# Performance work log

Hardware: AMD Instinct MI355X
Metric: run time of the kernel (lower is better)

The kernel has to match this reference:

```python
import jax, jax.numpy as jnp
import numpy as np

ANG = 5  # angRes; n = ANG*ANG
EPS = 1e-12  # torch F.normalize eps

def _l2norm(x, axis):
    n = jnp.sqrt(jnp.sum(x * x, axis=axis, keepdims=True))
    return x / jnp.maximum(n, EPS)

def setup_inputs() -> dict:
    key = jax.random.key(0)
    kq, kk, kv = jax.random.split(key, 3)
    shape = (16, 16, 25, 16, 128)  # b c n h w
    return {
        "token_q": jax.random.normal(kq, shape, dtype=jnp.float32),
        "token_k": jax.random.normal(kk, shape, dtype=jnp.float32),
        "token_v": jax.random.normal(kv, shape, dtype=jnp.float32),
    }

def reference(token_q, token_k, token_v):
    b, c, n, h, w = token_q.shape
    u = v = ANG
    buffer = token_v

    def to_q(x):  # b c (u v) h w -> b (c h) (w u v)
        return x.reshape(b, c, u, v, h, w).transpose(0, 1, 4, 5, 2, 3).reshape(b, c * h, w * u * v)

    def to_k(x):  # b c (u v) h w -> b (w u v) (c h)
        return x.reshape(b, c, u, v, h, w).transpose(0, 5, 2, 3, 1, 4).reshape(b, w * u * v, c * h)

    unfold_q = _l2norm(to_q(token_q), axis=-1)      # [b, ch, wuv]
    unfold_k = _l2norm(to_k(token_k), axis=-2)      # [b, wuv, ch]
    unfold_v = to_q(token_v)                        # [b, ch, wuv]

    att = jnp.einsum('bts,bsr->btr', unfold_q, unfold_k)  # [b, ch, ch]
    size = c * h
    causal = jnp.tril(jnp.ones((size, size), dtype=bool))
    att = jnp.where(causal, att, jnp.float32(-1e15))
    att = jax.nn.softmax(att, axis=-1)

    out = jnp.einsum('btr,brs->bts', att, unfold_v)  # [b, ch, wuv]
    # b (c h) (w u v) -> b c (u v) h w
    out = out.reshape(b, c, h, w, u, v).transpose(0, 1, 4, 5, 2, 3).reshape(b, c, n, h, w)
    return out + buffer
```

## Files before the change

kernel.cpp:

```cpp
#include <hip/hip_runtime.h>
#include <math.h>

#define SB 819200
#define SC 51200
#define SN 2048
#define CH 256
#define NW 3200
#define NPARTS 10
#define PARTLEN 320
#define SPART 1048576

typedef __bf16 bf16x8 __attribute__((ext_vector_type(8)));
typedef float  f32x4  __attribute__((ext_vector_type(4)));

__device__ __forceinline__ bf16x8 cvt8(float4 a, float4 b) {
    bf16x8 r;
    r[0] = (__bf16)a.x; r[1] = (__bf16)a.y; r[2] = (__bf16)a.z; r[3] = (__bf16)a.w;
    r[4] = (__bf16)b.x; r[5] = (__bf16)b.y; r[6] = (__bf16)b.z; r[7] = (__bf16)b.w;
    return r;
}

__global__ __launch_bounds__(256) void norms_kernel(const float* __restrict__ q,
                                                    const float* __restrict__ k,
                                                    float* __restrict__ inv_nq,
                                                    float* __restrict__ inv_nk) {
    const int row = blockIdx.x;
    const int b = row >> 8;
    const int t = row & 255;
    const size_t base = (size_t)b * SB + (size_t)(t >> 4) * SC + (size_t)(t & 15) * 128;
    const float* qb = q + base;
    const float* kb = k + base;

    float sq = 0.f, sk = 0.f;
#pragma unroll
    for (int it = 0; it < 4; it++) {
        const int f4 = threadIdx.x + it * 256;
        if (f4 < 800) {
            const int s = f4 * 4;
            const size_t off = (size_t)(s >> 7) * SN + (s & 127);
            const float4 a = *(const float4*)(qb + off);
            const float4 c = *(const float4*)(kb + off);
            sq += a.x * a.x + a.y * a.y + a.z * a.z + a.w * a.w;
            sk += c.x * c.x + c.y * c.y + c.z * c.z + c.w * c.w;
        }
    }
    __shared__ float redq[256];
    __shared__ float redk[256];
    redq[threadIdx.x] = sq;
    redk[threadIdx.x] = sk;
    __syncthreads();
    for (int off = 128; off > 0; off >>= 1) {
        if (threadIdx.x < off) {
            redq[threadIdx.x] += redq[threadIdx.x + off];
            redk[threadIdx.x] += redk[threadIdx.x + off];
        }
        __syncthreads();
    }
    if (threadIdx.x == 0) {
        inv_nq[row] = 1.0f / fmaxf(sqrtf(redq[0]), 1e-12f);
        inv_nk[row] = 1.0f / fmaxf(sqrtf(redk[0]), 1e-12f);
    }
}

__global__ __launch_bounds__(256, 2) void gemm1_kernel(const float* __restrict__ q,
                                                       const float* __restrict__ k,
                                                       float* __restrict__ Sp) {
    __shared__ alignas(16) __bf16 As[128 * 72];
    __shared__ alignas(16) __bf16 Bs[128 * 72];

    const int tid = threadIdx.x;
    const int b = blockIdx.z;
    const int part = blockIdx.y;
    const int tile = blockIdx.x;
    const int tm = (tile + 1) >> 1;
    const int tn = tile >> 1;

    const int lane = tid & 63;
    const int wave = tid >> 6;
    const int wm = wave >> 1;
    const int wn = wave & 1;

    const int srow = tid >> 1;
    const int scol = (tid & 1) * 32;
    const int ta = tm * 128 + srow;
    const int rb = tn * 128 + srow;
    const float* qrow = q + (size_t)b * SB + (size_t)(ta >> 4) * SC + (size_t)(ta & 15) * 128;
    const float* krow = k + (size_t)b * SB + (size_t)(rb >> 4) * SC + (size_t)(rb & 15) * 128;

    f32x4 acc[4][4] = {};
    bool live[4][4];
#pragma unroll
    for (int mi = 0; mi < 4; mi++)
#pragma unroll
        for (int ni = 0; ni < 4; ni++)
            live[mi][ni] = (tn * 128 + wn * 64 + ni * 16) <= (tm * 128 + wm * 64 + mi * 16);

    for (int ch = 0; ch < 5; ch++) {
        const int kg = part * PARTLEN + ch * 64;
        const size_t koff = (size_t)(kg >> 7) * SN + (kg & 127) + scol;

        float4 av[8], bv[8];
#pragma unroll
        for (int j = 0; j < 8; j++) {
            av[j] = *(const float4*)(qrow + koff + j * 4);
            bv[j] = *(const float4*)(krow + koff + j * 4);
        }
        __syncthreads();
#pragma unroll
        for (int j = 0; j < 4; j++) {
            *(bf16x8*)&As[srow * 72 + scol + j * 8] = cvt8(av[2 * j], av[2 * j + 1]);
            *(bf16x8*)&Bs[srow * 72 + scol + j * 8] = cvt8(bv[2 * j], bv[2 * j + 1]);
        }
        __syncthreads();
#pragma unroll
        for (int ks = 0; ks < 2; ks++) {
            const int ko = ks * 32 + (lane >> 4) * 8;
            bf16x8 af[4], bf[4];
#pragma unroll
            for (int mi = 0; mi < 4; mi++)
                af[mi] = *(const bf16x8*)&As[(wm * 64 + mi * 16 + (lane & 15)) * 72 + ko];
#pragma unroll
            for (int ni = 0; ni < 4; ni++)
                bf[ni] = *(const bf16x8*)&Bs[(wn * 64 + ni * 16 + (lane & 15)) * 72 + ko];
#pragma unroll
            for (int mi = 0; mi < 4; mi++)
#pragma unroll
                for (int ni = 0; ni < 4; ni++)
                    if (live[mi][ni])
                        acc[mi][ni] = __builtin_amdgcn_mfma_f32_16x16x32_bf16(
                            af[mi], bf[ni], acc[mi][ni], 0, 0, 0);
        }
    }

    float* o = Sp + (size_t)part * SPART + (size_t)b * 65536;
#pragma unroll
    for (int mi = 0; mi < 4; mi++)
#pragma unroll
        for (int ni = 0; ni < 4; ni++) {
            if (!live[mi][ni]) continue;
            const int r = tn * 128 + wn * 64 + ni * 16 + (lane & 15);
#pragma unroll
            for (int j = 0; j < 4; j++) {
                const int t = tm * 128 + wm * 64 + mi * 16 + (lane >> 4) * 4 + j;
                o[(size_t)t * 256 + r] = acc[mi][ni][j];
            }
        }
}

__global__ __launch_bounds__(256) void softmax_kernel(const float* __restrict__ Sp,
                                                      const float* __restrict__ inv_nq,
                                                      const float* __restrict__ inv_nk,
                                                      __bf16* __restrict__ P) {
    const int t = blockIdx.x;
    const int b = blockIdx.y;
    const int r = threadIdx.x;
    const size_t idx = ((size_t)b * 256 + t) * 256 + r;

    float val = -1e30f;
    if (r <= t) {
        float s = 0.f;
#pragma unroll
        for (int p = 0; p < NPARTS; p++) s += Sp[(size_t)p * SPART + idx];
        val = s * inv_nq[b * 256 + t] * inv_nk[b * 256 + r];
    }
    __shared__ float red[256];
    red[r] = val;
    __syncthreads();
    for (int off = 128; off > 0; off >>= 1) {
        if (r < off) red[r] = fmaxf(red[r], red[r + off]);
        __syncthreads();
    }
    const float m = red[0];
    __syncthreads();
    const float e = (r <= t) ? expf(val - m) : 0.f;
    red[r] = e;
    __syncthreads();
    for (int off = 128; off > 0; off >>= 1) {
        if (r < off) red[r] += red[r + off];
        __syncthreads();
    }
    P[idx] = (__bf16)(e / red[0]);
}

__global__ __launch_bounds__(256, 2) void gemm2_kernel(const __bf16* __restrict__ P,
                                                       const float* __restrict__ v,
                                                       float* __restrict__ out) {
    __shared__ alignas(16) __bf16 Ps[128 * 72];
    __shared__ alignas(16) __bf16 Vs[128 * 72];

    const int tid = threadIdx.x;
    const int b = blockIdx.z;
    const int tt = blockIdx.y;
    const int n = blockIdx.x;

    const int lane = tid & 63;
    const int wave = tid >> 6;
    const int wm = wave >> 1;
    const int wn = wave & 1;

    const int prow = tid >> 1;
    const int pcol = (tid & 1) * 32;
    const __bf16* Prow = P + ((size_t)b * 256 + tt * 128 + prow) * 256;

    const int vu = tid & 7;
    const int vr = tid >> 3;
    const float* vbase = v + (size_t)b * SB + (size_t)n * SN;

    f32x4 acc[4][4] = {};

    for (int kc = 0; kc < 4; kc++) {
        bf16x8 p4[4];
#pragma unroll
        for (int j = 0; j < 4; j++)
            p4[j] = *(const bf16x8*)(Prow + kc * 64 + pcol + j * 8);

        float4 vv[2][4];
#pragma unroll
        for (int g = 0; g < 2; g++) {
            const int rg = kc * 64 + vr + g * 32;
            const float* vrow = vbase + (size_t)(rg >> 4) * SC + (size_t)(rg & 15) * 128;
#pragma unroll
            for (int jj = 0; jj < 4; jj++)
                vv[g][jj] = *(const float4*)(vrow + vu * 16 + jj * 4);
        }
        __syncthreads();
#pragma unroll
        for (int j = 0; j < 4; j++)
            *(bf16x8*)&Ps[prow * 72 + pcol + j * 8] = p4[j];
#pragma unroll
        for (int g = 0; g < 2; g++) {
            const int rl = vr + g * 32;
            const int rsw = rl ^ (vu << 3);
#pragma unroll
            for (int jj = 0; jj < 4; jj++) {
                const float* f = (const float*)&vv[g][jj];
#pragma unroll
                for (int e = 0; e < 4; e++) {
                    const int s = vu * 16 + jj * 4 + e;
                    Vs[s * 72 + rsw] = (__bf16)f[e];
                }
            }
        }
        __syncthreads();
#pragma unroll
        for (int ks = 0; ks < 2; ks++) {
            const int ko = ks * 32 + (lane >> 4) * 8;
            bf16x8 af[4], bf[4];
#pragma unroll
            for (int mi = 0; mi < 4; mi++)
                af[mi] = *(const bf16x8*)&Ps[(wm * 64 + mi * 16 + (lane & 15)) * 72 + ko];
#pragma unroll
            for (int ni = 0; ni < 4; ni++) {
                const int s0 = wn * 64 + ni * 16;
                const int sw = ((s0 >> 4) & 7) << 3;
                bf[ni] = *(const bf16x8*)&Vs[(s0 + (lane & 15)) * 72 + (ko ^ sw)];
            }
#pragma unroll
            for (int mi = 0; mi < 4; mi++)
#pragma unroll
                for (int ni = 0; ni < 4; ni++)
                    acc[mi][ni] = __builtin_amdgcn_mfma_f32_16x16x32_bf16(
                        af[mi], bf[ni], acc[mi][ni], 0, 0, 0);
        }
        __syncthreads();
    }

#pragma unroll
    for (int mi = 0; mi < 4; mi++)
#pragma unroll
        for (int j = 0; j < 4; j++) {
            const int t = tt * 128 + wm * 64 + mi * 16 + (lane >> 4) * 4 + j;
            const size_t base = (size_t)b * SB + (size_t)(t >> 4) * SC +
                                (size_t)n * SN + (size_t)(t & 15) * 128;
#pragma unroll
            for (int ni = 0; ni < 4; ni++) {
                const int w = wn * 64 + ni * 16 + (lane & 15);
                const size_t a = base + w;
                out[a] = acc[mi][ni][j] + v[a];
            }
        }
}

extern "C" void kernel_launch(void* const* d_in, const int* in_sizes, int n_in,
                              void* d_out, int out_size, void* d_ws, size_t ws_size,
                              hipStream_t stream) {
    const float* q = (const float*)d_in[0];
    const float* k = (const float*)d_in[1];
    const float* v = (const float*)d_in[2];
    float* out = (float*)d_out;

    float* ws = (float*)d_ws;
    float* inv_nq = ws;
    float* inv_nk = ws + 4096;
    __bf16* P = (__bf16*)(ws + 8192);

    float* Spart = out;

    norms_kernel<<<dim3(4096), dim3(256), 0, stream>>>(q, k, inv_nq, inv_nk);
    gemm1_kernel<<<dim3(3, NPARTS, 16), dim3(256), 0, stream>>>(q, k, Spart);
    softmax_kernel<<<dim3(256, 16), dim3(256), 0, stream>>>(Spart, inv_nq, inv_nk, P);
    gemm2_kernel<<<dim3(25, 2, 16), dim3(256), 0, stream>>>(P, v, out);
}
```

Measured before the change: 243.0 us.

## Rework norms/softmax to wave-per-row, halve split-K parts, coalesce gemm2 epilogue

The norms and softmax kernels now assign one wave per row and reduce with shuffles instead of a shared-memory tree with many barriers. Softmax also reads vectorized float4 partials and writes bf16x4. gemm1 uses 5 split-K parts instead of 10, which halves partial-sum traffic but leaves fewer blocks in the grid. gemm2 stages its accumulators through shared memory so the residual add and output store use coalesced float4 accesses, and its launch bound is raised to 4 blocks per CU. The risks are lower gemm1 parallelism and extra barriers in the gemm2 epilogue.

```diff
diff --git a/kernel.cpp b/kernel.cpp
--- a/kernel.cpp
+++ b/kernel.cpp
@@ -6,11 +6,12 @@
 #define SN 2048
 #define CH 256
 #define NW 3200
-#define NPARTS 10
-#define PARTLEN 320
+#define NPARTS 5
+#define PARTLEN 640
 #define SPART 1048576
 
 typedef __bf16 bf16x8 __attribute__((ext_vector_type(8)));
+typedef __bf16 bf16x4 __attribute__((ext_vector_type(4)));
 typedef float  f32x4  __attribute__((ext_vector_type(4)));
 
 __device__ __forceinline__ bf16x8 cvt8(float4 a, float4 b) {
@@ -24,41 +25,29 @@
                                                     const float* __restrict__ k,
                                                     float* __restrict__ inv_nq,
                                                     float* __restrict__ inv_nk) {
-    const int row = blockIdx.x;
+    const int wave = threadIdx.x >> 6;
+    const int lane = threadIdx.x & 63;
+    const int row = blockIdx.x * 4 + wave;
     const int b = row >> 8;
     const int t = row & 255;
-    const size_t base = (size_t)b * SB + (size_t)(t >> 4) * SC + (size_t)(t & 15) * 128;
-    const float* qb = q + base;
-    const float* kb = k + base;
-
+    const size_t base = (size_t)b * SB + (size_t)(t >> 4) * SC +
+                        (size_t)(t & 15) * 128 + lane * 2;
     float sq = 0.f, sk = 0.f;
 #pragma unroll
-    for (int it = 0; it < 4; it++) {
-        const int f4 = threadIdx.x + it * 256;
-        if (f4 < 800) {
-            const int s = f4 * 4;
-            const size_t off = (size_t)(s >> 7) * SN + (s & 127);
-            const float4 a = *(const float4*)(qb + off);
-            const float4 c = *(const float4*)(kb + off);
-            sq += a.x * a.x + a.y * a.y + a.z * a.z + a.w * a.w;
-            sk += c.x * c.x + c.y * c.y + c.z * c.z + c.w * c.w;
-        }
-    }
-    __shared__ float redq[256];
-    __shared__ float redk[256];
-    redq[threadIdx.x] = sq;
-    redk[threadIdx.x] = sk;
-    __syncthreads();
-    for (int off = 128; off > 0; off >>= 1) {
-        if (threadIdx.x < off) {
-            redq[threadIdx.x] += redq[threadIdx.x + off];
-            redk[threadIdx.x] += redk[threadIdx.x + off];
-        }
-        __syncthreads();
-    }
-    if (threadIdx.x == 0) {
-        inv_nq[row] = 1.0f / fmaxf(sqrtf(redq[0]), 1e-12f);
-        inv_nk[row] = 1.0f / fmaxf(sqrtf(redk[0]), 1e-12f);
+    for (int nch = 0; nch < 25; nch++) {
+        const float2 a = *(const float2*)(q + base + (size_t)nch * SN);
+        const float2 c = *(const float2*)(k + base + (size_t)nch * SN);
+        sq += a.x * a.x + a.y * a.y;
+        sk += c.x * c.x + c.y * c.y;
+    }
+#pragma unroll
+    for (int off = 32; off; off >>= 1) {
+        sq += __shfl_xor(sq, off, 64);
+        sk += __shfl_xor(sk, off, 64);
+    }
+    if (lane == 0) {
+        inv_nq[row] = 1.0f / fmaxf(sqrtf(sq), 1e-12f);
+        inv_nk[row] = 1.0f / fmaxf(sqrtf(sk), 1e-12f);
     }
 }
 
@@ -95,7 +84,7 @@
         for (int ni = 0; ni < 4; ni++)
             live[mi][ni] = (tn * 128 + wn * 64 + ni * 16) <= (tm * 128 + wm * 64 + mi * 16);
 
-    for (int ch = 0; ch < 5; ch++) {
+    for (int ch = 0; ch < 10; ch++) {
         const int kg = part * PARTLEN + ch * 64;
         const size_t koff = (size_t)(kg >> 7) * SN + (kg & 127) + scol;
 
@@ -151,42 +140,58 @@
                                                       const float* __restrict__ inv_nq,
                                                       const float* __restrict__ inv_nk,
                                                       __bf16* __restrict__ P) {
-    const int t = blockIdx.x;
+    const int wave = threadIdx.x >> 6;
+    const int lane = threadIdx.x & 63;
+    const int t = blockIdx.x * 4 + wave;
     const int b = blockIdx.y;
-    const int r = threadIdx.x;
-    const size_t idx = ((size_t)b * 256 + t) * 256 + r;
-
-    float val = -1e30f;
-    if (r <= t) {
-        float s = 0.f;
-#pragma unroll
-        for (int p = 0; p < NPARTS; p++) s += Sp[(size_t)p * SPART + idx];
-        val = s * inv_nq[b * 256 + t] * inv_nk[b * 256 + r];
-    }
-    __shared__ float red[256];
-    red[r] = val;
-    __syncthreads();
-    for (int off = 128; off > 0; off >>= 1) {
-        if (r < off) red[r] = fmaxf(red[r], red[r + off]);
-        __syncthreads();
-    }
-    const float m = red[0];
-    __syncthreads();
-    const float e = (r <= t) ? expf(val - m) : 0.f;
-    red[r] = e;
-    __syncthreads();
-    for (int off = 128; off > 0; off >>= 1) {
-        if (r < off) red[r] += red[r + off];
-        __syncthreads();
-    }
-    P[idx] = (__bf16)(e / red[0]);
-}
-
-__global__ __launch_bounds__(256, 2) void gemm2_kernel(const __bf16* __restrict__ P,
+    const size_t rowbase = ((size_t)b * 256 + t) * 256;
+    const int r0 = lane * 4;
+
+    float4 s4 = {0.f, 0.f, 0.f, 0.f};
+#pragma unroll
+    for (int p = 0; p < NPARTS; p++) {
+        const float4 x = *(const float4*)(Sp + (size_t)p * SPART + rowbase + r0);
+        s4.x += x.x; s4.y += x.y; s4.z += x.z; s4.w += x.w;
+    }
+    const float qn = inv_nq[b * 256 + t];
+    const float4 kn = *(const float4*)(inv_nk + b * 256 + r0);
+
+    float val[4] = {s4.x * qn * kn.x, s4.y * qn * kn.y,
+                    s4.z * qn * kn.z, s4.w * qn * kn.w};
+    float m = -1e30f;
+#pragma unroll
+    for (int j = 0; j < 4; j++) {
+        if (r0 + j > t) val[j] = -1e30f;
+        m = fmaxf(m, val[j]);
+    }
+#pragma unroll
+    for (int off = 32; off; off >>= 1) m = fmaxf(m, __shfl_xor(m, off, 64));
+
+    float e[4], sum = 0.f;
+#pragma unroll
+    for (int j = 0; j < 4; j++) {
+        e[j] = (r0 + j <= t) ? expf(val[j] - m) : 0.f;
+        sum += e[j];
+    }
+#pragma unroll
+    for (int off = 32; off; off >>= 1) sum += __shfl_xor(sum, off, 64);
+
+    const float inv = 1.0f / sum;
+    bf16x4 o;
+    o[0] = (__bf16)(e[0] * inv);
+    o[1] = (__bf16)(e[1] * inv);
+    o[2] = (__bf16)(e[2] * inv);
+    o[3] = (__bf16)(e[3] * inv);
+    *(bf16x4*)(P + rowbase + r0) = o;
+}
+
+__global__ __launch_bounds__(256, 4) void gemm2_kernel(const __bf16* __restrict__ P,
                                                        const float* __restrict__ v,
                                                        float* __restrict__ out) {
-    __shared__ alignas(16) __bf16 Ps[128 * 72];
-    __shared__ alignas(16) __bf16 Vs[128 * 72];
+    __shared__ alignas(16) char smem[36864];
+    __bf16* Ps = (__bf16*)smem;
+    __bf16* Vs = (__bf16*)(smem + 18432);
+    float* Es = (float*)smem;
 
     const int tid = threadIdx.x;
     const int b = blockIdx.z;
@@ -265,20 +270,34 @@
         __syncthreads();
     }
 
-#pragma unroll
-    for (int mi = 0; mi < 4; mi++)
-#pragma unroll
-        for (int j = 0; j < 4; j++) {
-            const int t = tt * 128 + wm * 64 + mi * 16 + (lane >> 4) * 4 + j;
-            const size_t base = (size_t)b * SB + (size_t)(t >> 4) * SC +
-                                (size_t)n * SN + (size_t)(t & 15) * 128;
-#pragma unroll
-            for (int ni = 0; ni < 4; ni++) {
-                const int w = wn * 64 + ni * 16 + (lane & 15);
-                const size_t a = base + w;
-                out[a] = acc[mi][ni][j] + v[a];
-            }
-        }
+    for (int half = 0; half < 2; half++) {
+        if (half == 1) __syncthreads();
+        if (wm == half) {
+#pragma unroll
+            for (int mi = 0; mi < 4; mi++)
+#pragma unroll
+                for (int ni = 0; ni < 4; ni++)
+#pragma unroll
+                    for (int j = 0; j < 4; j++) {
+                        const int trow = mi * 16 + (lane >> 4) * 4 + j;
+                        const int wcol = wn * 64 + ni * 16 + (lane & 15);
+                        Es[trow * 132 + wcol] = acc[mi][ni][j];
+                    }
+        }
+        __syncthreads();
+#pragma unroll
+        for (int it = 0; it < 8; it++) {
+            const int tl = it * 8 + (tid >> 5);
+            const int w4 = (tid & 31) * 4;
+            const int t = tt * 128 + half * 64 + tl;
+            const size_t a = (size_t)b * SB + (size_t)(t >> 4) * SC + (size_t)n * SN +
+                             (size_t)(t & 15) * 128 + w4;
+            float4 r4 = *(const float4*)&Es[tl * 132 + w4];
+            const float4 buf = *(const float4*)(v + a);
+            r4.x += buf.x; r4.y += buf.y; r4.z += buf.z; r4.w += buf.w;
+            *(float4*)(out + a) = r4;
+        }
+    }
 }
 
 extern "C" void kernel_launch(void* const* d_in, const int* in_sizes, int n_in,
@@ -296,8 +315,8 @@
 
     float* Spart = out;
 
-    norms_kernel<<<dim3(4096), dim3(256), 0, stream>>>(q, k, inv_nq, inv_nk);
+    norms_kernel<<<dim3(1024), dim3(256), 0, stream>>>(q, k, inv_nq, inv_nk);
     gemm1_kernel<<<dim3(3, NPARTS, 16), dim3(256), 0, stream>>>(q, k, Spart);
-    softmax_kernel<<<dim3(256, 16), dim3(256), 0, stream>>>(Spart, inv_nq, inv_nk, P);
+    softmax_kernel<<<dim3(64, 16), dim3(256), 0, stream>>>(Spart, inv_nq, inv_nk, P);
     gemm2_kernel<<<dim3(25, 2, 16), dim3(256), 0, stream>>>(P, v, out);
 }
```

Result: no change. 246.6 us (+1.5%).
